# Kernel tuning notes

Measured on AMD Instinct MI355X. Metric: run time of the kernel, lower is better.

Reference implementation:

```python
import jax, jax.numpy as jnp
import numpy as np

SR = 22050
HOP = 512
N_FFT = 2048
N_BINS = 84
BPO = 12
FMIN = 27.5


def setup_inputs() -> dict:
    key = jax.random.key(0)
    audio = jax.random.normal(key, (16, 1310720), dtype=jnp.float32)
    return {"audio": audio}


def _stft_magnitude(audio):
    # torch.stft defaults: center=True, pad_mode='reflect', onesided, not normalized
    pad = N_FFT // 2
    x = jnp.pad(audio, ((0, 0), (pad, pad)), mode="reflect")  # (B, S + n_fft)
    n_frames = 1 + audio.shape[1] // HOP
    # frame indices: (T, n_fft)
    idx = jnp.arange(n_frames)[:, None] * HOP + jnp.arange(N_FFT)[None, :]
    frames = x[:, idx]  # (B, T, n_fft)
    # periodic Hann window (torch.hann_window default)
    n = jnp.arange(N_FFT, dtype=jnp.float32)
    window = 0.5 * (1.0 - jnp.cos(2.0 * jnp.pi * n / N_FFT))
    spec = jnp.fft.rfft(frames * window, axis=-1)  # (B, T, F=1025)
    return jnp.abs(spec)


def reference(audio):
    mag = _stft_magnitude(audio)  # (B, T, F)
    stft_freqs = jnp.fft.rfftfreq(N_FFT, 1.0 / SR).astype(jnp.float32)  # (F,)
    cqt_freqs = FMIN * 2.0 ** (jnp.arange(N_BINS, dtype=jnp.float32) / BPO)  # (K,)
    # Precompute Gaussian-like weights as a single (K, F) basis matrix
    freq_diff = jnp.abs(stft_freqs[None, :] - cqt_freqs[:, None])
    weights = jnp.exp(-freq_diff / (cqt_freqs[:, None] * 0.1))  # (K, F)
    # Per-bin weighted sum over frequency == one GEMM-style contraction
    cqt = jnp.einsum("kf,btf->bkt", weights, mag)  # (B, K, T)
    return jnp.log10(cqt + 1e-10)
```

## Files before the change

kernel.cpp:

```cpp
#include <hip/hip_runtime.h>
#include <hip/hip_bf16.h>
#include <math.h>

#define AUDIO_LEN 1310720
#define NBATCH    16
#define NFRAMES   2561
#define NT        (NBATCH * NFRAMES)
#define NFFT      2048
#define HALF_N    1024
#define NK        84
#define NF        1025
#define MROW      1056
#define NCH       33

#define TW_OFF   0
#define WIN_OFF  2052
#define WF_OFF   4104
#define MAG_OFF_B 294912

typedef _Float16 h8    __attribute__((ext_vector_type(8)));
typedef float    f32x4 __attribute__((ext_vector_type(4)));
typedef float    f2    __attribute__((ext_vector_type(2)));
typedef float    f4    __attribute__((ext_vector_type(4)));

__device__ __forceinline__ void gll16(const void* src, void* dst) {
    __builtin_amdgcn_global_load_lds(
        (const __attribute__((address_space(1))) void*)src,
        (__attribute__((address_space(3))) void*)dst, 16, 0, 0);
}

__device__ __forceinline__ f2 cmul(f2 a, f2 b) {
    f2 t = a.yy * b.yx;
    f2 m; m.x = -t.x; m.y = t.y;
    return a.xx * b + m;
}

#define DFT4V(p0, p1, p2, p3, y0, y1, y2, y3) do {                       \
    const f2 u0 = (p0) + (p2), u1 = (p0) - (p2);                         \
    const f2 u2 = (p1) + (p3), u3 = (p1) - (p3);                         \
    f2 r; r.x = u3.y; r.y = -u3.x;                          \
    (y0) = u0 + u2; (y2) = u0 - u2;                                      \
    (y1) = u1 + r;  (y3) = u1 - r;                                       \
} while (0)

__device__ __forceinline__ void dft16v(f2* v) {
    const float C = 0.92387953251128674f;
    const float S = 0.38268343236508978f;
    const float H = 0.70710678118654752f;
    const f2 W1 = {C, -S}, W2c = {H, -H}, W3 = {S, -C}, W6 = {-H, -H}, W9 = {-C, S};
    f2 A[16];
#pragma unroll
    for (int b = 0; b < 4; b++)
        DFT4V(v[b], v[b + 4], v[b + 8], v[b + 12],
              A[b * 4 + 0], A[b * 4 + 1], A[b * 4 + 2], A[b * 4 + 3]);
    A[5]  = cmul(A[5],  W1);
    A[6]  = cmul(A[6],  W2c);
    A[7]  = cmul(A[7],  W3);
    A[9]  = cmul(A[9],  W2c);
    { f2 r; r.x = A[10].y; r.y = -A[10].x; A[10] = r; }
    A[11] = cmul(A[11], W6);
    A[13] = cmul(A[13], W3);
    A[14] = cmul(A[14], W6);
    A[15] = cmul(A[15], W9);
#pragma unroll
    for (int d1 = 0; d1 < 4; d1++)
        DFT4V(A[0 + d1], A[4 + d1], A[8 + d1], A[12 + d1],
              v[d1], v[d1 + 4], v[d1 + 8], v[d1 + 12]);
}

__device__ __forceinline__ void twiddle15v(f2* v, f2 w1) {
    f2 wp[16];
    wp[1]  = w1;
    wp[2]  = cmul(w1, w1);
    wp[3]  = cmul(wp[2], w1);
    wp[4]  = cmul(wp[2], wp[2]);
    wp[5]  = cmul(wp[4], w1);
    wp[6]  = cmul(wp[3], wp[3]);
    wp[7]  = cmul(wp[4], wp[3]);
    wp[8]  = cmul(wp[4], wp[4]);
    wp[9]  = cmul(wp[8], w1);
    wp[10] = cmul(wp[5], wp[5]);
    wp[11] = cmul(wp[8], wp[3]);
    wp[12] = cmul(wp[6], wp[6]);
    wp[13] = cmul(wp[8], wp[5]);
    wp[14] = cmul(wp[7], wp[7]);
    wp[15] = cmul(wp[8], wp[7]);
#pragma unroll
    for (int i = 1; i < 16; i++) v[i] = cmul(v[i], wp[i]);
}

__global__ __launch_bounds__(256) void init_tables_kernel(float* __restrict__ ws) {
    int i = blockIdx.x * 256 + threadIdx.x;
    if (i < NCH * 512 * 8) {
        int i8 = i & 7;
        int c  = i >> 3;
        int ck = c >> 9;
        int cc = c & 511;
        int mt = cc >> 6;
        int l  = cc & 63;
        int k  = mt * 16 + (l & 15);
        int f  = ck * 32 + (l >> 4) * 8 + i8;
        float w = 0.0f;
        if (cc < 384 && k < NK && f < NF) {
            float sf = (float)f * (22050.0f / 2048.0f);
            float cf = 27.5f * exp2f((float)k * (1.0f / 12.0f));
            w = expf(-fabsf(sf - cf) / (0.1f * cf));
        }
        ((_Float16*)(ws + WF_OFF))[i] = (_Float16)w;
    }
    if (i <= HALF_N) {
        double ang = -2.0 * M_PI * (double)i / 2048.0;
        ws[TW_OFF + 2 * i]     = (float)cos(ang);
        ws[TW_OFF + 2 * i + 1] = (float)sin(ang);
    }
    if (i < NFFT) {
        double ang = 2.0 * M_PI * (double)i / 2048.0;
        ws[WIN_OFF + i] = (float)(0.5 * (1.0 - cos(ang)));
    }
}

__global__ __launch_bounds__(128) void fft_kernel(const float* __restrict__ audio,
                                                  const float* __restrict__ ws,
                                                  _Float16* __restrict__ mag) {
    __shared__ f2 Abuf[2][HALF_N];

    const int t    = threadIdx.x & 63;
    const int wave = threadIdx.x >> 6;
    const int ft   = blockIdx.x * 2 + wave;
    const int b    = ft / NFRAMES;
    const int tf   = ft - b * NFRAMES;
    f2* __restrict__ A = Abuf[wave];

    const f2* __restrict__ TWv = (const f2*)(ws + TW_OFF);
    const f2* __restrict__ W2v = (const f2*)(ws + WIN_OFF);
    const float* __restrict__ ab = audio + (size_t)b * AUDIO_LEN;
    const int base = tf * 512 - 1024;

    const f2 wtree0 = TWv[2 * t];
    const f2 wtree1 = TWv[32 * (t >> 4)];
    const f2 wt     = TWv[t];

    f2 x[16];
    if (tf >= 2 && tf <= 2558) {
        const f2* __restrict__ a2 = (const f2*)(ab + base);
#pragma unroll
        for (int l = 0; l < 16; l++) {
            const int p = t + 64 * l;
            x[l] = a2[p] * W2v[p];
        }
    } else {
#pragma unroll
        for (int l = 0; l < 16; l++) {
            const int p = t + 64 * l;
            int j0 = base + 2 * p, j1 = j0 + 1;
            j0 = (j0 < 0) ? -j0 : ((j0 >= AUDIO_LEN) ? 2 * AUDIO_LEN - 2 - j0 : j0);
            j1 = (j1 < 0) ? -j1 : ((j1 >= AUDIO_LEN) ? 2 * AUDIO_LEN - 2 - j1 : j1);
            f2 v; v.x = ab[j0]; v.y = ab[j1];
            x[l] = v * W2v[p];
        }
    }

    dft16v(x);
    twiddle15v(x, wtree0);
    {
        f4* A4 = (f4*)A;
        const int m = (t ^ (t >> 3)) & 7;
#pragma unroll
        for (int dp = 0; dp < 8; dp++)
            A4[8 * t + (dp ^ m)] = __builtin_shufflevector(x[2 * dp], x[2 * dp + 1], 0, 1, 2, 3);
    }

    int adr[16];
#pragma unroll
    for (int s = 0; s < 16; s++) {
        const int p = t + 64 * s;
        adr[s] = p ^ (((((p >> 4) ^ (p >> 7)) & 7)) << 1);
    }

#pragma unroll
    for (int l = 0; l < 16; l++) x[l] = A[adr[l]];
    dft16v(x);
    twiddle15v(x, wtree1);
    {
        const int basei = (t & 15) + 256 * (t >> 4);
#pragma unroll
        for (int d = 0; d < 16; d++) {
            const int p = basei + 16 * d;
            A[p ^ (((((p >> 4) ^ (p >> 7)) & 7)) << 1)] = x[d];
        }
    }

#pragma unroll
    for (int s = 0; s < 16; s++) x[s] = A[adr[s]];
    f2 xf[16];
#pragma unroll
    for (int w = 0; w < 4; w++)
        DFT4V(x[w], x[w + 4], x[w + 8], x[w + 12],
              xf[w], xf[w + 4], xf[w + 8], xf[w + 12]);

    const float CS[16] = { 1.0f,               0.98078528040323f,  0.92387953251129f,  0.83146961230255f,
                           0.70710678118655f,  0.55557023301960f,  0.38268343236509f,  0.19509032201613f,
                           0.0f,              -0.19509032201613f, -0.38268343236509f, -0.55557023301960f,
                          -0.70710678118655f, -0.83146961230255f, -0.92387953251129f, -0.98078528040323f };
    const float SN[16] = { 0.0f,               0.19509032201613f,  0.38268343236509f,  0.55557023301960f,
                           0.70710678118655f,  0.83146961230255f,  0.92387953251129f,  0.98078528040323f,
                           1.0f,               0.98078528040323f,  0.92387953251129f,  0.83146961230255f,
                           0.70710678118655f,  0.55557023301960f,  0.38268343236509f,  0.19509032201613f };

    const int src = (64 - t) & 63;
    f2 rt; rt.x = wt.y; rt.y = -wt.x;
    _Float16* __restrict__ mrow = mag + (size_t)ft * MROW;
#pragma unroll
    for (int s = 0; s < 16; s++) {
        float ux = __shfl(xf[15 - s].x, src, 64);
        float uy = __shfl(xf[15 - s].y, src, 64);
        if (t == 0) { ux = xf[(16 - s) & 15].x; uy = xf[(16 - s) & 15].y; }
        const f2 z = xf[s];
        f2 cu; cu.x = ux; cu.y = -uy;
        const f2 a = z + cu;
        const f2 d = z - cu;
        f2 pp; pp.x = d.y; pp.y = -d.x;
        const f2 wk = wt * CS[s] + rt * SN[s];
        const f2 Y = a + cmul(wk, pp);
        mrow[t + 64 * s] = (_Float16)(0.5f * sqrtf(fmaf(Y.x, Y.x, Y.y * Y.y)));
    }
    if (t == 0) mrow[1024] = (_Float16)fabsf(xf[0].x - xf[0].y);
    if (t < MROW - NF) mrow[NF + t] = (_Float16)0.0f;
}

__global__ __launch_bounds__(256) void proj_kernel(const float* __restrict__ ws,
                                                   const _Float16* __restrict__ mag,
                                                   float* __restrict__ out) {
    __shared__ __align__(16) _Float16 As[2][4096];
    __shared__ __align__(16) _Float16 Bs[2][4096];

    const int tid  = threadIdx.x;
    const int lane = tid & 63;
    const int w    = tid >> 6;
    const int ft0  = blockIdx.x * 128;

    const _Float16* __restrict__ wf = (const _Float16*)(ws + WF_OFF);

    const int fr = tid >> 2, kg = tid & 3;
    int ftc0 = ft0 + fr;       if (ftc0 >= NT) ftc0 = NT - 1;
    int ftc1 = ft0 + fr + 64;  if (ftc1 >= NT) ftc1 = NT - 1;
    const _Float16* bsrc0 = mag + (size_t)ftc0 * MROW + kg * 8;
    const _Float16* bsrc1 = mag + (size_t)ftc1 * MROW + kg * 8;

#define STAGE(nb, ck)  do {                                                   \
        const _Float16* asrc = wf + (size_t)(ck) * 4096;                      \
        gll16(asrc + (size_t)tid * 8,         &As[nb][tid * 8]);              \
        gll16(asrc + (size_t)(tid + 256) * 8, &As[nb][(tid + 256) * 8]);      \
        gll16(bsrc0 + (ck) * 32,              &Bs[nb][tid * 8]);              \
        gll16(bsrc1 + (ck) * 32,              &Bs[nb][(tid + 256) * 8]);      \
    } while (0)

    f32x4 acc[6][2];
#pragma unroll
    for (int mt = 0; mt < 6; mt++)
#pragma unroll
        for (int nt = 0; nt < 2; nt++) acc[mt][nt] = (f32x4)0.0f;

    STAGE(0, 0);
    int cur = 0;
    for (int ck = 0; ck < NCH; ck++) {
        if (ck + 1 < NCH) {
            STAGE(cur ^ 1, ck + 1);
            asm volatile("s_waitcnt vmcnt(4)" ::: "memory");
        } else {
            asm volatile("s_waitcnt vmcnt(0)" ::: "memory");
        }
        __builtin_amdgcn_s_barrier();

        h8 a[6], bb[2];
#pragma unroll
        for (int mt = 0; mt < 6; mt++)
            a[mt] = *(const h8*)&As[cur][(mt * 64 + lane) * 8];
#pragma unroll
        for (int nt = 0; nt < 2; nt++) {
            const int slot = (w * 32 + nt * 16 + (lane & 15)) * 4 + (lane >> 4);
            bb[nt] = *(const h8*)&Bs[cur][slot * 8];
        }
#pragma unroll
        for (int mt = 0; mt < 6; mt++)
#pragma unroll
            for (int nt = 0; nt < 2; nt++)
                acc[mt][nt] = __builtin_amdgcn_mfma_f32_16x16x32_f16(a[mt], bb[nt], acc[mt][nt], 0, 0, 0);

        asm volatile("" ::: "memory");
        __builtin_amdgcn_s_barrier();
        cur ^= 1;
    }
#undef STAGE

    const int fcol = lane & 15, frow = lane >> 4;
#pragma unroll
    for (int nt = 0; nt < 2; nt++) {
        const int ft = ft0 + w * 32 + nt * 16 + fcol;
        if (ft < NT) {
            const int b = ft / NFRAMES;
            const int t = ft - b * NFRAMES;
#pragma unroll
            for (int mt = 0; mt < 6; mt++)
#pragma unroll
                for (int r = 0; r < 4; r++) {
                    const int k = mt * 16 + frow * 4 + r;
                    if (k < NK)
                        out[((size_t)b * NK + k) * NFRAMES + t] = log10f(acc[mt][nt][r] + 1e-10f);
                }
        }
    }
}

extern "C" void kernel_launch(void* const* d_in, const int* in_sizes, int n_in,
                              void* d_out, int out_size, void* d_ws, size_t ws_size,
                              hipStream_t stream) {
    const float* audio = (const float*)d_in[0];
    float* out = (float*)d_out;
    float* ws  = (float*)d_ws;
    _Float16* mag = (_Float16*)((char*)d_ws + MAG_OFF_B);

    hipLaunchKernelGGL(init_tables_kernel, dim3(528), dim3(256), 0, stream, ws);
    hipLaunchKernelGGL(fft_kernel, dim3(NT / 2), dim3(128), 0, stream, audio, ws, mag);
    hipLaunchKernelGGL(proj_kernel, dim3((NT + 127) / 128), dim3(256), 0, stream, ws, mag, out);
}
```

Measured before the change: 130.7 us.

## Make FFT kernel persistent with hoisted twiddle trees and folded window scale

The FFT kernel now launches a fixed grid of 1536 blocks, and each wave loops over frames with a grid stride instead of handling one frame per wave. The per-thread twiddle power trees and constants are built once and reused across all frames that wave processes. The 0.5 output scale is folded into the window table (0.25 instead of 0.5), so the per-bin multiply disappears. An explicit lgkmcnt wait and a sched_barrier guard LDS reuse across loop iterations. In exchange, the hoisted twiddles raise register pressure, which may lower occupancy or hurt latency hiding.

```diff
diff --git a/kernel.cpp b/kernel.cpp
--- a/kernel.cpp
+++ b/kernel.cpp
@@ -13,6 +13,9 @@
 #define MROW      1056
 #define NCH       33
 
+#define FFT_BLOCKS 1536
+#define NWAVES     (FFT_BLOCKS * 2)
+
 #define TW_OFF   0
 #define WIN_OFF  2052
 #define WF_OFF   4104
@@ -21,7 +24,6 @@
 typedef _Float16 h8    __attribute__((ext_vector_type(8)));
 typedef float    f32x4 __attribute__((ext_vector_type(4)));
 typedef float    f2    __attribute__((ext_vector_type(2)));
-typedef float    f4    __attribute__((ext_vector_type(4)));
 
 __device__ __forceinline__ void gll16(const void* src, void* dst) {
     __builtin_amdgcn_global_load_lds(
@@ -68,8 +70,7 @@
               v[d1], v[d1 + 4], v[d1 + 8], v[d1 + 12]);
 }
 
-__device__ __forceinline__ void twiddle15v(f2* v, f2 w1) {
-    f2 wp[16];
+__device__ __forceinline__ void build_tree(f2* wp, f2 w1) {
     wp[1]  = w1;
     wp[2]  = cmul(w1, w1);
     wp[3]  = cmul(wp[2], w1);
@@ -85,8 +86,6 @@
     wp[13] = cmul(wp[8], wp[5]);
     wp[14] = cmul(wp[7], wp[7]);
     wp[15] = cmul(wp[8], wp[7]);
-#pragma unroll
-    for (int i = 1; i < 16; i++) v[i] = cmul(v[i], wp[i]);
 }
 
 __global__ __launch_bounds__(256) void init_tables_kernel(float* __restrict__ ws) {
@@ -115,7 +114,7 @@
     }
     if (i < NFFT) {
         double ang = 2.0 * M_PI * (double)i / 2048.0;
-        ws[WIN_OFF + i] = (float)(0.5 * (1.0 - cos(ang)));
+        ws[WIN_OFF + i] = (float)(0.25 * (1.0 - cos(ang)));
     }
 }
 
@@ -126,77 +125,24 @@
 
     const int t    = threadIdx.x & 63;
     const int wave = threadIdx.x >> 6;
-    const int ft   = blockIdx.x * 2 + wave;
-    const int b    = ft / NFRAMES;
-    const int tf   = ft - b * NFRAMES;
     f2* __restrict__ A = Abuf[wave];
 
     const f2* __restrict__ TWv = (const f2*)(ws + TW_OFF);
     const f2* __restrict__ W2v = (const f2*)(ws + WIN_OFF);
-    const float* __restrict__ ab = audio + (size_t)b * AUDIO_LEN;
-    const int base = tf * 512 - 1024;
-
-    const f2 wtree0 = TWv[2 * t];
-    const f2 wtree1 = TWv[32 * (t >> 4)];
-    const f2 wt     = TWv[t];
-
-    f2 x[16];
-    if (tf >= 2 && tf <= 2558) {
-        const f2* __restrict__ a2 = (const f2*)(ab + base);
-#pragma unroll
-        for (int l = 0; l < 16; l++) {
-            const int p = t + 64 * l;
-            x[l] = a2[p] * W2v[p];
-        }
-    } else {
-#pragma unroll
-        for (int l = 0; l < 16; l++) {
-            const int p = t + 64 * l;
-            int j0 = base + 2 * p, j1 = j0 + 1;
-            j0 = (j0 < 0) ? -j0 : ((j0 >= AUDIO_LEN) ? 2 * AUDIO_LEN - 2 - j0 : j0);
-            j1 = (j1 < 0) ? -j1 : ((j1 >= AUDIO_LEN) ? 2 * AUDIO_LEN - 2 - j1 : j1);
-            f2 v; v.x = ab[j0]; v.y = ab[j1];
-            x[l] = v * W2v[p];
-        }
-    }
-
-    dft16v(x);
-    twiddle15v(x, wtree0);
-    {
-        f4* A4 = (f4*)A;
-        const int m = (t ^ (t >> 3)) & 7;
-#pragma unroll
-        for (int dp = 0; dp < 8; dp++)
-            A4[8 * t + (dp ^ m)] = __builtin_shufflevector(x[2 * dp], x[2 * dp + 1], 0, 1, 2, 3);
-    }
-
+
+    f2 wp0[16], wp1[16];
+    build_tree(wp0, TWv[2 * t]);
+    build_tree(wp1, TWv[32 * (t >> 4)]);
+    const f2 wt = TWv[t];
+    f2 rt; rt.x = wt.y; rt.y = -wt.x;
     int adr[16];
 #pragma unroll
     for (int s = 0; s < 16; s++) {
         const int p = t + 64 * s;
         adr[s] = p ^ (((((p >> 4) ^ (p >> 7)) & 7)) << 1);
     }
-
-#pragma unroll
-    for (int l = 0; l < 16; l++) x[l] = A[adr[l]];
-    dft16v(x);
-    twiddle15v(x, wtree1);
-    {
-        const int basei = (t & 15) + 256 * (t >> 4);
-#pragma unroll
-        for (int d = 0; d < 16; d++) {
-            const int p = basei + 16 * d;
-            A[p ^ (((((p >> 4) ^ (p >> 7)) & 7)) << 1)] = x[d];
-        }
-    }
-
-#pragma unroll
-    for (int s = 0; s < 16; s++) x[s] = A[adr[s]];
-    f2 xf[16];
-#pragma unroll
-    for (int w = 0; w < 4; w++)
-        DFT4V(x[w], x[w + 4], x[w + 8], x[w + 12],
-              xf[w], xf[w + 4], xf[w + 8], xf[w + 12]);
+    const int src   = (64 - t) & 63;
+    const int m_swz = (t ^ (t >> 3)) & 7;
 
     const float CS[16] = { 1.0f,               0.98078528040323f,  0.92387953251129f,  0.83146961230255f,
                            0.70710678118655f,  0.55557023301960f,  0.38268343236509f,  0.19509032201613f,
@@ -207,25 +153,88 @@
                            1.0f,               0.98078528040323f,  0.92387953251129f,  0.83146961230255f,
                            0.70710678118655f,  0.55557023301960f,  0.38268343236509f,  0.19509032201613f };
 
-    const int src = (64 - t) & 63;
-    f2 rt; rt.x = wt.y; rt.y = -wt.x;
-    _Float16* __restrict__ mrow = mag + (size_t)ft * MROW;
-#pragma unroll
-    for (int s = 0; s < 16; s++) {
-        float ux = __shfl(xf[15 - s].x, src, 64);
-        float uy = __shfl(xf[15 - s].y, src, 64);
-        if (t == 0) { ux = xf[(16 - s) & 15].x; uy = xf[(16 - s) & 15].y; }
-        const f2 z = xf[s];
-        f2 cu; cu.x = ux; cu.y = -uy;
-        const f2 a = z + cu;
-        const f2 d = z - cu;
-        f2 pp; pp.x = d.y; pp.y = -d.x;
-        const f2 wk = wt * CS[s] + rt * SN[s];
-        const f2 Y = a + cmul(wk, pp);
-        mrow[t + 64 * s] = (_Float16)(0.5f * sqrtf(fmaf(Y.x, Y.x, Y.y * Y.y)));
-    }
-    if (t == 0) mrow[1024] = (_Float16)fabsf(xf[0].x - xf[0].y);
-    if (t < MROW - NF) mrow[NF + t] = (_Float16)0.0f;
+    for (int ft = blockIdx.x * 2 + wave; ft < NT; ft += NWAVES) {
+        const int b  = ft / NFRAMES;
+        const int tf = ft - b * NFRAMES;
+        const float* __restrict__ ab = audio + (size_t)b * AUDIO_LEN;
+        const int base = tf * 512 - 1024;
+
+        f2 x[16];
+        if (tf >= 2 && tf <= 2558) {
+            const f2* __restrict__ a2 = (const f2*)(ab + base);
+#pragma unroll
+            for (int l = 0; l < 16; l++) {
+                const int p = t + 64 * l;
+                x[l] = a2[p] * W2v[p];
+            }
+        } else {
+#pragma unroll
+            for (int l = 0; l < 16; l++) {
+                const int p = t + 64 * l;
+                int j0 = base + 2 * p, j1 = j0 + 1;
+                j0 = (j0 < 0) ? -j0 : ((j0 >= AUDIO_LEN) ? 2 * AUDIO_LEN - 2 - j0 : j0);
+                j1 = (j1 < 0) ? -j1 : ((j1 >= AUDIO_LEN) ? 2 * AUDIO_LEN - 2 - j1 : j1);
+                f2 v; v.x = ab[j0]; v.y = ab[j1];
+                x[l] = v * W2v[p];
+            }
+        }
+
+        dft16v(x);
+#pragma unroll
+        for (int i = 1; i < 16; i++) x[i] = cmul(x[i], wp0[i]);
+
+        asm volatile("s_waitcnt lgkmcnt(0)" ::: "memory");
+        __builtin_amdgcn_sched_barrier(0);
+
+        {
+            const int bi = 16 * t;
+#pragma unroll
+            for (int dp = 0; dp < 8; dp++) {
+                const int q = bi + 2 * (dp ^ m_swz);
+                A[q]     = x[2 * dp];
+                A[q + 1] = x[2 * dp + 1];
+            }
+        }
+
+#pragma unroll
+        for (int l = 0; l < 16; l++) x[l] = A[adr[l]];
+        dft16v(x);
+#pragma unroll
+        for (int i = 1; i < 16; i++) x[i] = cmul(x[i], wp1[i]);
+        {
+            const int basei = (t & 15) + 256 * (t >> 4);
+#pragma unroll
+            for (int d = 0; d < 16; d++) {
+                const int p = basei + 16 * d;
+                A[p ^ (((((p >> 4) ^ (p >> 7)) & 7)) << 1)] = x[d];
+            }
+        }
+
+#pragma unroll
+        for (int s = 0; s < 16; s++) x[s] = A[adr[s]];
+#pragma unroll
+        for (int w = 0; w < 4; w++)
+            DFT4V(x[w], x[w + 4], x[w + 8], x[w + 12],
+                  x[w], x[w + 4], x[w + 8], x[w + 12]);
+
+        _Float16* __restrict__ mrow = mag + (size_t)ft * MROW;
+#pragma unroll
+        for (int s = 0; s < 16; s++) {
+            float ux = __shfl(x[15 - s].x, src, 64);
+            float uy = __shfl(x[15 - s].y, src, 64);
+            if (t == 0) { ux = x[(16 - s) & 15].x; uy = x[(16 - s) & 15].y; }
+            const f2 z = x[s];
+            f2 cu; cu.x = ux; cu.y = -uy;
+            const f2 a = z + cu;
+            const f2 d = z - cu;
+            f2 pp; pp.x = d.y; pp.y = -d.x;
+            const f2 wk = wt * CS[s] + rt * SN[s];
+            const f2 Y = a + cmul(wk, pp);
+            mrow[t + 64 * s] = (_Float16)sqrtf(fmaf(Y.x, Y.x, Y.y * Y.y));
+        }
+        if (t == 0) mrow[1024] = (_Float16)(2.0f * fabsf(x[0].x - x[0].y));
+        if (t < MROW - NF) mrow[NF + t] = (_Float16)0.0f;
+    }
 }
 
 __global__ __launch_bounds__(256) void proj_kernel(const float* __restrict__ ws,
@@ -321,6 +330,6 @@
     _Float16* mag = (_Float16*)((char*)d_ws + MAG_OFF_B);
 
     hipLaunchKernelGGL(init_tables_kernel, dim3(528), dim3(256), 0, stream, ws);
-    hipLaunchKernelGGL(fft_kernel, dim3(NT / 2), dim3(128), 0, stream, audio, ws, mag);
+    hipLaunchKernelGGL(fft_kernel, dim3(FFT_BLOCKS), dim3(128), 0, stream, audio, ws, mag);
     hipLaunchKernelGGL(proj_kernel, dim3((NT + 127) / 128), dim3(256), 0, stream, ws, mag, out);
 }
```

Result: slower. 344.7 us (+163.7%).
